# Optimization experiments

Measured on AMD Instinct MI355X. Metric: run time of the kernel, lower is better.

## Reference

```python
import jax, jax.numpy as jnp
import numpy as np

BN_EPS = 1e-5

def _conv(x, w, b, pad):
    # x: [B,C,H,W], w: [O,I,kh,kw] -> [B,O,H,W]
    y = jax.lax.conv_general_dilated(x, w, window_strides=(1, 1),
                                     padding=[(pad, pad), (pad, pad)],
                                     dimension_numbers=("NCHW", "OIHW", "NCHW"))
    return y + b[None, :, None, None]

def setup_inputs() -> dict:
    key = jax.random.key(0)
    ks = jax.random.split(key, 5)
    B, Cin, H, W = 2, 256, 80, 80
    Ck, Cv, Cout = 128, 256, 256
    std = 0.02  # matches torch normal_(0, 0.02) init
    return {
        "x": jax.random.normal(ks[0], (B, Cin, H, W), jnp.float32),
        "wk": std * jax.random.normal(ks[1], (Ck, Cin, 1, 1), jnp.float32),
        "bk": jnp.zeros((Ck,), jnp.float32),
        "gamma": jnp.ones((Ck,), jnp.float32),
        "beta": jnp.zeros((Ck,), jnp.float32),
        "rmean": jnp.zeros((Ck,), jnp.float32),
        "rvar": jnp.ones((Ck,), jnp.float32),
        "wv": std * jax.random.normal(ks[2], (Cv, Cin, 3, 3), jnp.float32),
        "bv": jnp.zeros((Cv,), jnp.float32),
        "ww": std * jax.random.normal(ks[3], (Cout, Cv, 1, 1), jnp.float32),
        "bw": jnp.zeros((Cout,), jnp.float32),
    }

def reference(x, wk, bk, gamma, beta, rmean, rvar, wv, bv, ww, bw):
    B, Cin, H, W = x.shape
    Ck, Cv = wk.shape[0], wv.shape[0]
    N = H * W

    # f_key == f_query (shared module): 1x1 conv + BatchNorm (inference stats)
    kq = _conv(x, wk, bk, pad=0)                      # [B,Ck,H,W]
    inv = gamma / jnp.sqrt(rvar + BN_EPS)
    kq = kq * inv[None, :, None, None] + (beta - rmean * inv)[None, :, None, None]
    kq = kq.reshape(B, Ck, N)                          # key layout [B,Ck,N]

    # f_value: 3x3 conv
    value = _conv(x, wv, bv, pad=1).reshape(B, Cv, N)  # [B,Cv,N]

    # sim_map = query^T @ key -> [B,N,N], full softmax over last dim
    sim = jnp.einsum("bcn,bcm->bnm", kq, kq)
    sim = jax.nn.softmax(sim, axis=-1)

    # context = sim @ value^T -> [B,N,Cv] -> [B,Cv,H,W]
    ctx = jnp.einsum("bnm,bcm->bcn", sim, value).reshape(B, Cv, H, W)

    out = _conv(ctx, ww, bw, pad=0) + x                # residual
    return out
```

## Files before the change

kernel.cpp:

```cpp
#include <hip/hip_runtime.h>
#include <math.h>

#define NB   2
#define CIN  256
#define IMH  80
#define IMW  80
#define NPIX (IMH*IMW)
#define CK   128
#define CVC  256
#define COUTC 256
#define BN_EPS 1e-5f
#define HP   82
#define WP   82
#define NMC  (NPIX / 64)
#define LOG2E 1.4426950408889634f
#define M0L  28.853900817779268f

typedef short sx8 __attribute__((ext_vector_type(8)));
typedef short sx4 __attribute__((ext_vector_type(4)));
typedef float f32x4 __attribute__((ext_vector_type(4)));

__device__ __forceinline__ short f2bf(float f) {
    unsigned u = __builtin_bit_cast(unsigned, f);
    u += 0x7fffu + ((u >> 16) & 1u);
    return (short)(u >> 16);
}
__device__ __forceinline__ float bf2f(short s) {
    unsigned u = ((unsigned)(unsigned short)s) << 16;
    return __builtin_bit_cast(float, u);
}
__device__ __forceinline__ int pk_bf16(float a, float b) {
    unsigned ua = __builtin_bit_cast(unsigned, a) + 0x8000u;
    unsigned ub = __builtin_bit_cast(unsigned, b) + 0x8000u;
    return __builtin_amdgcn_perm(ub, ua, 0x07060302);
}

#define WVT_BLKS 256
#define WWB_BLKS 256
#define WKB_BLKS 128
__global__ __launch_bounds__(256) void prep_kernel(
    const float* __restrict__ wv, const float* __restrict__ ww,
    const float* __restrict__ wk, const float* __restrict__ bk,
    const float* __restrict__ gamma, const float* __restrict__ beta,
    const float* __restrict__ rmean, const float* __restrict__ rvar,
    short* __restrict__ wvt, short* __restrict__ wwb,
    short* __restrict__ wkb, float* __restrict__ bias2)
{
    __shared__ short L[9][258];
    const int tid = threadIdx.x;
    const int bx  = blockIdx.x;

    if (bx < WVT_BLKS) {
        const float* src = wv + (size_t)bx * 2304;
        #pragma unroll
        for (int i = 0; i < 9; ++i) {
            int m = i * 256 + tid;
            L[m % 9][m / 9] = f2bf(src[m]);
        }
        __syncthreads();
        #pragma unroll
        for (int j = 0; j < 9; ++j)
            wvt[(size_t)j * (CVC * CIN) + bx * 256 + tid] = L[j][tid];
    } else if (bx < WVT_BLKS + WWB_BLKS) {
        int idx = (bx - WVT_BLKS) * 256 + tid;
        wwb[idx] = f2bf(ww[idx]);
    } else {
        int idx = (bx - WVT_BLKS - WWB_BLKS) * 256 + tid;
        int ck = idx >> 8;
        float inv = gamma[ck] * rsqrtf(rvar[ck] + BN_EPS);
        wkb[idx] = f2bf(wk[idx] * inv);
        if (idx < CK) {
            float invi = gamma[idx] * rsqrtf(rvar[idx] + BN_EPS);
            bias2[idx] = (bk[idx] - rmean[idx]) * invi + beta[idx];
        }
    }
}

__global__ __launch_bounds__(256) void padkq_kernel(
    const float* __restrict__ x, const short* __restrict__ wkb,
    const float* __restrict__ bias2, short* __restrict__ xpad,
    short* __restrict__ kqT)
{
    __shared__ short T[64][258];
    const int tid = threadIdx.x;
    const int n0  = blockIdx.x * 64;
    const int b   = blockIdx.y;
    const float* xb = x + (size_t)b * CIN * NPIX;

    #pragma unroll 4
    for (int i = 0; i < 64; ++i) {
        int e = tid + i * 256;
        int pix = e & 63, c = e >> 6;
        T[pix][c] = f2bf(xb[(size_t)c * NPIX + n0 + pix]);
    }
    __syncthreads();

    #pragma unroll
    for (int i = 0; i < 8; ++i) {
        int e   = tid + i * 256;
        int pix = e >> 5;
        int cp  = (e & 31) * 8;
        int np  = n0 + pix;
        int hp  = np / IMW + 1, wp = np % IMW + 1;
        sx8 v = *(const sx8*)&T[pix][cp];
        *(sx8*)&xpad[(((size_t)b * HP + hp) * WP + wp) * CIN + cp] = v;
    }

    {
        int e = blockIdx.x * 256 + tid;
        if (e < 324 * 32) {
            int p = e >> 5, c8 = (e & 31) * 8;
            int hp, wp;
            if      (p < 82)  { hp = 0;       wp = p;       }
            else if (p < 164) { hp = 81;      wp = p - 82;  }
            else if (p < 244) { hp = p - 163; wp = 0;       }
            else              { hp = p - 243; wp = 81;      }
            sx8 z = {};
            *(sx8*)&xpad[(((size_t)b * HP + hp) * WP + wp) * CIN + c8] = z;
        }
    }

    const int wid  = tid >> 6;
    const int lane = tid & 63;
    const int l15  = lane & 15;
    const int quad = lane >> 4;
    const int ck0  = wid * 32;

    f32x4 acc[2][4];
    #pragma unroll
    for (int at = 0; at < 2; ++at)
        #pragma unroll
        for (int nt = 0; nt < 4; ++nt)
            acc[at][nt] = (f32x4){0.f, 0.f, 0.f, 0.f};

    for (int kc = 0; kc < CIN / 32; ++kc) {
        sx8 af0 = *(const sx8*)&wkb[(size_t)(ck0 + l15) * CIN + kc * 32 + quad * 8];
        sx8 af1 = *(const sx8*)&wkb[(size_t)(ck0 + 16 + l15) * CIN + kc * 32 + quad * 8];
        #pragma unroll
        for (int nt = 0; nt < 4; ++nt) {
            sx8 bf = *(const sx8*)&T[nt * 16 + l15][kc * 32 + quad * 8];
            acc[0][nt] = __builtin_amdgcn_mfma_f32_16x16x32_bf16(af0, bf, acc[0][nt], 0, 0, 0);
            acc[1][nt] = __builtin_amdgcn_mfma_f32_16x16x32_bf16(af1, bf, acc[1][nt], 0, 0, 0);
        }
    }

    __syncthreads();

    #pragma unroll
    for (int at = 0; at < 2; ++at) {
        f32x4 b4 = *(const f32x4*)&bias2[ck0 + at * 16 + quad * 4];
        #pragma unroll
        for (int nt = 0; nt < 4; ++nt)
            #pragma unroll
            for (int r = 0; r < 4; ++r)
                T[nt * 16 + l15][ck0 + at * 16 + quad * 4 + r] = f2bf(acc[at][nt][r] + b4[r]);
    }
    __syncthreads();
    #pragma unroll
    for (int it = 0; it < 4; ++it) {
        int e = tid + it * 256;
        int row = e >> 4, c8 = (e & 15) * 8;
        *(sx8*)&kqT[((size_t)b * NPIX + n0 + row) * CK + c8] = *(const sx8*)&T[row][c8];
    }
}

#define CSTRIDE 36
__global__ __launch_bounds__(512) void conv3_kernel(
    const short* __restrict__ xpad, const short* __restrict__ wvt,
    const float* __restrict__ bv, short* __restrict__ valF)
{
    __shared__ __align__(16) short Xs[2][6 * 18 * CSTRIDE];

    const int tid  = threadIdx.x;
    const int wid  = tid >> 6;
    const int lane = tid & 63;
    const int l15  = lane & 15;
    const int quad = lane >> 4;

    const int rowT = blockIdx.x / 5, colT = blockIdx.x % 5;
    const int h0 = rowT * 4, w0 = colT * 16;
    const int cv0 = blockIdx.y * 128 + wid * 16;
    const int b   = blockIdx.z;

    const short* xb = xpad + (size_t)b * HP * WP * CIN;

    const int rc  = tid >> 2, l4 = tid & 3;
    const int row = rc / 18, col = rc % 18;
    const bool sv = (tid < 432);
    const short* sptr = &xb[(((size_t)(h0 + row)) * WP + (w0 + col)) * CIN + l4 * 8];
    const int sdst = rc * CSTRIDE + l4 * 8;

    f32x4 acc[4];
    #pragma unroll
    for (int r = 0; r < 4; ++r) acc[r] = (f32x4){0.f, 0.f, 0.f, 0.f};

    sx8 v = {};
    if (sv) {
        v = *(const sx8*)&sptr[0];
        *(sx8*)&Xs[0][sdst] = v;
    }
    __syncthreads();

    for (int cc = 0; cc < CIN / 32; ++cc) {
        const int cur = cc & 1;
        if (cc + 1 < CIN / 32 && sv)
            v = *(const sx8*)&sptr[(cc + 1) * 32];

        #pragma unroll
        for (int dw = 0; dw < 3; ++dw) {
            sx8 Bf[6];
            #pragma unroll
            for (int rr = 0; rr < 6; ++rr)
                Bf[rr] = *(const sx8*)&Xs[cur][(rr * 18 + l15 + dw) * CSTRIDE + quad * 8];
            #pragma unroll
            for (int dh = 0; dh < 3; ++dh) {
                int tap = dh * 3 + dw;
                sx8 Af = *(const sx8*)&wvt[((size_t)(tap * 256 + cv0 + l15)) * CIN + cc * 32 + quad * 8];
                #pragma unroll
                for (int r = 0; r < 4; ++r)
                    acc[r] = __builtin_amdgcn_mfma_f32_16x16x32_bf16(Af, Bf[r + dh], acc[r], 0, 0, 0);
            }
        }

        if (cc + 1 < CIN / 32 && sv)
            *(sx8*)&Xs[cur ^ 1][sdst] = v;
        __syncthreads();
    }

    f32x4 bvv = *(const f32x4*)&bv[cv0 + quad * 4];
    const int cvt = cv0 >> 4;
    #pragma unroll
    for (int r = 0; r < 4; ++r) {
        int n  = (h0 + r) * IMW + w0 + l15;
        int mc = n >> 6, s2 = (n >> 5) & 1, qm = (n >> 3) & 3, mi = n & 7;
        size_t base = ((((size_t)(b * NMC + mc) * 16 + cvt) * 2 + s2) * 4 + qm) * 128;
        #pragma unroll
        for (int reg = 0; reg < 4; ++reg)
            valF[base + (quad * 4 + reg) * 8 + mi] = f2bf(acc[r][reg] + bvv[reg]);
    }
}

#define TQ 64
#define TK 64
#define KS_LD 132
#define PS_LD 72

template<int SP>
__global__ __launch_bounds__(512) void attn_kernel(
    const short* __restrict__ kqT, const short* __restrict__ valF,
    short* __restrict__ opart, float* __restrict__ lpart)
{
    constexpr int NCc  = NPIX / SP / 64;
    constexpr int SPSH = (SP == 4) ? 3 : 2;

    __shared__ __align__(16) short Ks[TK][KS_LD];
    __shared__ __align__(16) short Pb[TQ][PS_LD];
    __shared__ float lqs[2][64];

    const int tid  = threadIdx.x;
    const int wid  = tid >> 6;
    const int lane = tid & 63;
    const int l15  = lane & 15;
    const int quad = lane >> 4;
    const int qw   = wid & 3;
    const int mh   = wid >> 2;

    const int blk = blockIdx.x;
    const int b   = blk & 1;
    const int sp  = (blk >> 1) & (SP - 1);
    const int n0  = (blk >> SPSH) * TQ;
    const int mb  = sp * (NPIX / SP);

    const short* kqb = kqT + (size_t)b * NPIX * CK;
    const short* vbase = valF + ((size_t)(b * NMC + sp * NCc) * 16 + wid * 2) * 1024
                              + (size_t)lane * 8;

    const int srow = tid >> 4;
    const int sc8  = (tid & 15) * 8;

    sx8 qf[4];
    #pragma unroll
    for (int s = 0; s < 4; ++s)
        qf[s] = *(const sx8*)&kqb[(size_t)(n0 + qw * 16 + l15) * CK + s * 32 + quad * 8];

    sx8 kreg[2];
    #pragma unroll
    for (int p = 0; p < 2; ++p)
        kreg[p] = *(const sx8*)&kqb[(size_t)(mb + srow + p * 32) * CK + sc8];
    #pragma unroll
    for (int p = 0; p < 2; ++p)
        *(sx8*)&Ks[srow + p * 32][sc8] = kreg[p];

    sx8 vreg[4];
    #pragma unroll
    for (int ct = 0; ct < 2; ++ct)
        #pragma unroll
        for (int s2 = 0; s2 < 2; ++s2)
            vreg[ct * 2 + s2] = *(const sx8*)&vbase[ct * 1024 + s2 * 512];

    float lq = 0.f;
    f32x4 acc[4][2];
    #pragma unroll
    for (int qt = 0; qt < 4; ++qt)
        #pragma unroll
        for (int ct = 0; ct < 2; ++ct)
            acc[qt][ct] = (f32x4){0.f, 0.f, 0.f, 0.f};

    __syncthreads();

    for (int i = 0; i < NCc; ++i) {
        if (i + 1 < NCc) {
            #pragma unroll
            for (int p = 0; p < 2; ++p)
                kreg[p] = *(const sx8*)&kqb[(size_t)(mb + (i + 1) * TK + srow + p * 32) * CK + sc8];
        }

        f32x4 st[2];
        #pragma unroll
        for (int t2 = 0; t2 < 2; ++t2) st[t2] = (f32x4){0.f, 0.f, 0.f, 0.f};
        #pragma unroll
        for (int s = 0; s < 4; ++s) {
            sx8 af[2];
            #pragma unroll
            for (int t2 = 0; t2 < 2; ++t2)
                af[t2] = *(const sx8*)&Ks[mh * 32 + t2 * 16 + l15][s * 32 + quad * 8];
            #pragma unroll
            for (int t2 = 0; t2 < 2; ++t2)
                st[t2] = __builtin_amdgcn_mfma_f32_16x16x32_bf16(af[t2], qf[s], st[t2], 0, 0, 0);
        }

        __syncthreads();

        #pragma unroll
        for (int t2 = 0; t2 < 2; ++t2)
            #pragma unroll
            for (int r = 0; r < 4; ++r)
                st[t2][r] = exp2f(fmaf(st[t2][r], LOG2E, -M0L));

        if (i + 1 < NCc) {
            #pragma unroll
            for (int p = 0; p < 2; ++p)
                *(sx8*)&Ks[srow + p * 32][sc8] = kreg[p];
        }

        #pragma unroll
        for (int t2 = 0; t2 < 2; ++t2) {
            int2 pw;
            pw.x = pk_bf16(st[t2][0], st[t2][1]);
            pw.y = pk_bf16(st[t2][2], st[t2][3]);
            *(int2*)&Pb[qw * 16 + l15][mh * 32 + t2 * 16 + quad * 4] = pw;
        }

        lq += (st[0][0] + st[0][1]) + (st[0][2] + st[0][3])
            + (st[1][0] + st[1][1]) + (st[1][2] + st[1][3]);

        __syncthreads();

        #pragma unroll
        for (int s2 = 0; s2 < 2; ++s2) {
            sx8 pa[4];
            #pragma unroll
            for (int qt = 0; qt < 4; ++qt)
                pa[qt] = *(const sx8*)&Pb[qt * 16 + l15][s2 * 32 + quad * 8];
            #pragma unroll
            for (int ct = 0; ct < 2; ++ct) {
                #pragma unroll
                for (int qt = 0; qt < 4; ++qt)
                    acc[qt][ct] = __builtin_amdgcn_mfma_f32_16x16x32_bf16(pa[qt], vreg[ct * 2 + s2], acc[qt][ct], 0, 0, 0);
            }
        }

        if (i + 1 < NCc) {
            #pragma unroll
            for (int ct = 0; ct < 2; ++ct)
                #pragma unroll
                for (int s2 = 0; s2 < 2; ++s2)
                    vreg[ct * 2 + s2] = *(const sx8*)&vbase[(size_t)(i + 1) * 16384 + ct * 1024 + s2 * 512];
        }
    }

    lq += __shfl_xor(lq, 16);
    lq += __shfl_xor(lq, 32);
    if (quad == 0)
        lqs[mh][qw * 16 + l15] = lq;

    size_t obase = (size_t)(sp * NB + b) * NPIX + n0;
    #pragma unroll
    for (int qt = 0; qt < 4; ++qt)
        #pragma unroll
        for (int ct = 0; ct < 2; ++ct) {
            int cv = wid * 32 + ct * 16 + l15;
            #pragma unroll
            for (int r = 0; r < 4; ++r)
                opart[(obase + qt * 16 + quad * 4 + r) * CVC + cv] = f2bf(acc[qt][ct][r]);
        }

    __syncthreads();
    if (tid < 64)
        lpart[obase + tid] = lqs[0][tid] + lqs[1][tid];
}

#define BS_LD 40
template<int SP>
__global__ __launch_bounds__(512) void out_kernel(
    const short* __restrict__ opart, const float* __restrict__ lpart,
    const short* __restrict__ wwb, const float* __restrict__ bw,
    const float* __restrict__ x, float* __restrict__ out)
{
    __shared__ __align__(16) short Bs[2][64][BS_LD];
    __shared__ float rinvs[64];

    const int tid  = threadIdx.x;
    const int wid  = tid >> 6;
    const int lane = tid & 63;
    const int l15  = lane & 15;
    const int quad = lane >> 4;

    const int n0  = blockIdx.x * 64;
    const int co0 = wid * 32;
    const int b   = blockIdx.y;

    if (tid < 64) {
        int n = n0 + tid;
        float ls = 0.f;
        #pragma unroll
        for (int s = 0; s < SP; ++s)
            ls += lpart[(size_t)(s * NB + b) * NPIX + n];
        rinvs[tid] = 1.f / ls;
    }

    const int srow = tid >> 2;
    const int sc8  = (tid & 3) * 8;
    const short* op0 = opart + ((size_t)b * NPIX + n0 + srow) * CVC + sc8;
    constexpr size_t SSTR = (size_t)NB * NPIX * CVC;
    const bool sv = (tid < 256);

    __syncthreads();

    if (sv) {
        float ri = rinvs[srow];
        float sacc[8] = {0.f, 0.f, 0.f, 0.f, 0.f, 0.f, 0.f, 0.f};
        #pragma unroll
        for (int s = 0; s < SP; ++s) {
            sx8 a = *(const sx8*)&op0[s * SSTR];
            #pragma unroll
            for (int j = 0; j < 8; ++j)
                sacc[j] += bf2f(a[j]);
        }
        sx8 o;
        #pragma unroll
        for (int j = 0; j < 8; ++j)
            o[j] = f2bf(sacc[j] * ri);
        *(sx8*)&Bs[0][srow][sc8] = o;
    }
    __syncthreads();

    f32x4 acc[4][2];
    #pragma unroll
    for (int nt = 0; nt < 4; ++nt)
        #pragma unroll
        for (int ct = 0; ct < 2; ++ct)
            acc[nt][ct] = (f32x4){0.f, 0.f, 0.f, 0.f};

    for (int cc = 0; cc < CVC / 32; ++cc) {
        const int cur = cc & 1;
        const bool st = (cc + 1 < CVC / 32) && sv;

        sx8 a[SP];
        if (st) {
            #pragma unroll
            for (int s = 0; s < SP; ++s)
                a[s] = *(const sx8*)&op0[s * SSTR + (cc + 1) * 32];
        }

        sx8 af[2];
        #pragma unroll
        for (int ct = 0; ct < 2; ++ct)
            af[ct] = *(const sx8*)&wwb[(size_t)(co0 + ct * 16 + l15) * CVC + cc * 32 + quad * 8];
        #pragma unroll
        for (int nt = 0; nt < 4; ++nt) {
            sx8 bf = *(const sx8*)&Bs[cur][nt * 16 + l15][quad * 8];
            #pragma unroll
            for (int ct = 0; ct < 2; ++ct)
                acc[nt][ct] = __builtin_amdgcn_mfma_f32_16x16x32_bf16(af[ct], bf, acc[nt][ct], 0, 0, 0);
        }

        if (st) {
            float ri = rinvs[srow];
            float sacc[8] = {0.f, 0.f, 0.f, 0.f, 0.f, 0.f, 0.f, 0.f};
            #pragma unroll
            for (int s = 0; s < SP; ++s)
                #pragma unroll
                for (int j = 0; j < 8; ++j)
                    sacc[j] += bf2f(a[s][j]);
            sx8 o;
            #pragma unroll
            for (int j = 0; j < 8; ++j)
                o[j] = f2bf(sacc[j] * ri);
            *(sx8*)&Bs[cur ^ 1][srow][sc8] = o;
        }
        __syncthreads();
    }

    #pragma unroll
    for (int ct = 0; ct < 2; ++ct) {
        f32x4 bv4 = *(const f32x4*)&bw[co0 + ct * 16 + quad * 4];
        #pragma unroll
        for (int nt = 0; nt < 4; ++nt) {
            #pragma unroll
            for (int r = 0; r < 4; ++r) {
                int co = co0 + ct * 16 + quad * 4 + r;
                int n  = n0 + nt * 16 + l15;
                size_t gi = ((size_t)b * COUTC + co) * NPIX + n;
                out[gi] = acc[nt][ct][r] + bv4[r] + x[gi];
            }
        }
    }
}

extern "C" void kernel_launch(void* const* d_in, const int* in_sizes, int n_in,
                              void* d_out, int out_size, void* d_ws, size_t ws_size,
                              hipStream_t stream)
{
    const float* x     = (const float*)d_in[0];
    const float* wk    = (const float*)d_in[1];
    const float* bk    = (const float*)d_in[2];
    const float* gamma = (const float*)d_in[3];
    const float* beta  = (const float*)d_in[4];
    const float* rmean = (const float*)d_in[5];
    const float* rvar  = (const float*)d_in[6];
    const float* wv    = (const float*)d_in[7];
    const float* bv    = (const float*)d_in[8];
    const float* ww    = (const float*)d_in[9];
    const float* bw    = (const float*)d_in[10];
    float* out = (float*)d_out;

    constexpr int SPL = 2;
    const size_t perSplit = (size_t)NB * NPIX * CVC;

    short* opart = (short*)d_ws;
    short* xpad  = opart;
    short* wvt   = xpad + (size_t)NB * HP * WP * CIN;
    short* wwb   = opart + (size_t)SPL * perSplit;
    short* wkb   = wwb  + (size_t)COUTC * CVC;
    short* kqT   = wkb  + (size_t)CK * CIN;
    short* valF  = kqT  + (size_t)NB * NPIX * CK;
    float* bias2 = (float*)(valF + perSplit);
    float* lpart = bias2 + CK;

    prep_kernel  <<<WVT_BLKS + WWB_BLKS + WKB_BLKS, 256, 0, stream>>>(
        wv, ww, wk, bk, gamma, beta, rmean, rvar, wvt, wwb, wkb, bias2);
    padkq_kernel <<<dim3(NPIX/64, NB),          256, 0, stream>>>(x, wkb, bias2, xpad, kqT);
    conv3_kernel <<<dim3(100, CVC/128,     NB), 512, 0, stream>>>(xpad, wvt, bv, valF);
    attn_kernel<SPL> <<<NB * SPL * (NPIX / TQ), 512, 0, stream>>>(kqT, valF, opart, lpart);
    out_kernel<SPL>  <<<dim3(100, NB),          512, 0, stream>>>(opart, lpart, wwb, bw, x, out);
}
```

Baseline: 223.8 us.

## Double attention query tile to 128 with 1024-thread blocks and 4-way key split

The attention kernel now processes 128 queries per block with 16 waves. Each wave owns 16 value channels instead of 32, and the key dimension is split into 4 partitions instead of 2. Doubling the query tile halves the number of times K and V tiles are re-read per query, while the larger split keeps the block count up. The cost is more partial outputs for out_kernel to reduce, larger 1024-thread blocks with tighter register limits, and more partial-result memory traffic. The workspace layout must also hold 4 splits, and it is unclear that it does.

After: 253.4 us. 1.13x slower.

```diff
diff --git a/kernel.cpp b/kernel.cpp
--- a/kernel.cpp
+++ b/kernel.cpp
@@ -240,13 +240,13 @@
     }
 }
 
-#define TQ 64
+#define TQ 128
 #define TK 64
 #define KS_LD 132
 #define PS_LD 72
 
 template<int SP>
-__global__ __launch_bounds__(512) void attn_kernel(
+__global__ __launch_bounds__(1024) void attn_kernel(
     const short* __restrict__ kqT, const short* __restrict__ valF,
     short* __restrict__ opart, float* __restrict__ lpart)
 {
@@ -255,15 +255,15 @@
 
     __shared__ __align__(16) short Ks[TK][KS_LD];
     __shared__ __align__(16) short Pb[TQ][PS_LD];
-    __shared__ float lqs[2][64];
+    __shared__ float lqs[2][TQ];
 
     const int tid  = threadIdx.x;
     const int wid  = tid >> 6;
     const int lane = tid & 63;
     const int l15  = lane & 15;
     const int quad = lane >> 4;
-    const int qw   = wid & 3;
-    const int mh   = wid >> 2;
+    const int qw   = wid & 7;
+    const int mh   = wid >> 3;
 
     const int blk = blockIdx.x;
     const int b   = blk & 1;
@@ -272,7 +272,7 @@
     const int mb  = sp * (NPIX / SP);
 
     const short* kqb = kqT + (size_t)b * NPIX * CK;
-    const short* vbase = valF + ((size_t)(b * NMC + sp * NCc) * 16 + wid * 2) * 1024
+    const short* vbase = valF + ((size_t)(b * NMC + sp * NCc) * 16 + wid) * 1024
                               + (size_t)lane * 8;
 
     const int srow = tid >> 4;
@@ -283,37 +283,25 @@
     for (int s = 0; s < 4; ++s)
         qf[s] = *(const sx8*)&kqb[(size_t)(n0 + qw * 16 + l15) * CK + s * 32 + quad * 8];
 
-    sx8 kreg[2];
-    #pragma unroll
-    for (int p = 0; p < 2; ++p)
-        kreg[p] = *(const sx8*)&kqb[(size_t)(mb + srow + p * 32) * CK + sc8];
-    #pragma unroll
-    for (int p = 0; p < 2; ++p)
-        *(sx8*)&Ks[srow + p * 32][sc8] = kreg[p];
-
-    sx8 vreg[4];
-    #pragma unroll
-    for (int ct = 0; ct < 2; ++ct)
-        #pragma unroll
-        for (int s2 = 0; s2 < 2; ++s2)
-            vreg[ct * 2 + s2] = *(const sx8*)&vbase[ct * 1024 + s2 * 512];
+    sx8 kreg = *(const sx8*)&kqb[(size_t)(mb + srow) * CK + sc8];
+    *(sx8*)&Ks[srow][sc8] = kreg;
+
+    sx8 vreg[2];
+    #pragma unroll
+    for (int s2 = 0; s2 < 2; ++s2)
+        vreg[s2] = *(const sx8*)&vbase[s2 * 512];
 
     float lq = 0.f;
-    f32x4 acc[4][2];
-    #pragma unroll
-    for (int qt = 0; qt < 4; ++qt)
-        #pragma unroll
-        for (int ct = 0; ct < 2; ++ct)
-            acc[qt][ct] = (f32x4){0.f, 0.f, 0.f, 0.f};
+    f32x4 acc[8];
+    #pragma unroll
+    for (int qt = 0; qt < 8; ++qt)
+        acc[qt] = (f32x4){0.f, 0.f, 0.f, 0.f};
 
     __syncthreads();
 
     for (int i = 0; i < NCc; ++i) {
-        if (i + 1 < NCc) {
-            #pragma unroll
-            for (int p = 0; p < 2; ++p)
-                kreg[p] = *(const sx8*)&kqb[(size_t)(mb + (i + 1) * TK + srow + p * 32) * CK + sc8];
-        }
+        if (i + 1 < NCc)
+            kreg = *(const sx8*)&kqb[(size_t)(mb + (i + 1) * TK + srow) * CK + sc8];
 
         f32x4 st[2];
         #pragma unroll
@@ -337,11 +325,8 @@
             for (int r = 0; r < 4; ++r)
                 st[t2][r] = exp2f(fmaf(st[t2][r], LOG2E, -M0L));
 
-        if (i + 1 < NCc) {
-            #pragma unroll
-            for (int p = 0; p < 2; ++p)
-                *(sx8*)&Ks[srow + p * 32][sc8] = kreg[p];
-        }
+        if (i + 1 < NCc)
+            *(sx8*)&Ks[srow][sc8] = kreg;
 
         #pragma unroll
         for (int t2 = 0; t2 < 2; ++t2) {
@@ -358,24 +343,19 @@
 
         #pragma unroll
         for (int s2 = 0; s2 < 2; ++s2) {
-            sx8 pa[4];
-            #pragma unroll
-            for (int qt = 0; qt < 4; ++qt)
+            sx8 pa[8];
+            #pragma unroll
+            for (int qt = 0; qt < 8; ++qt)
                 pa[qt] = *(const sx8*)&Pb[qt * 16 + l15][s2 * 32 + quad * 8];
             #pragma unroll
-            for (int ct = 0; ct < 2; ++ct) {
-                #pragma unroll
-                for (int qt = 0; qt < 4; ++qt)
-                    acc[qt][ct] = __builtin_amdgcn_mfma_f32_16x16x32_bf16(pa[qt], vreg[ct * 2 + s2], acc[qt][ct], 0, 0, 0);
-            }
+            for (int qt = 0; qt < 8; ++qt)
+                acc[qt] = __builtin_amdgcn_mfma_f32_16x16x32_bf16(pa[qt], vreg[s2], acc[qt], 0, 0, 0);
         }
 
         if (i + 1 < NCc) {
             #pragma unroll
-            for (int ct = 0; ct < 2; ++ct)
-                #pragma unroll
-                for (int s2 = 0; s2 < 2; ++s2)
-                    vreg[ct * 2 + s2] = *(const sx8*)&vbase[(size_t)(i + 1) * 16384 + ct * 1024 + s2 * 512];
+            for (int s2 = 0; s2 < 2; ++s2)
+                vreg[s2] = *(const sx8*)&vbase[(size_t)(i + 1) * 16384 + s2 * 512];
         }
     }
 
@@ -385,18 +365,16 @@
         lqs[mh][qw * 16 + l15] = lq;
 
     size_t obase = (size_t)(sp * NB + b) * NPIX + n0;
-    #pragma unroll
-    for (int qt = 0; qt < 4; ++qt)
-        #pragma unroll
-        for (int ct = 0; ct < 2; ++ct) {
-            int cv = wid * 32 + ct * 16 + l15;
-            #pragma unroll
-            for (int r = 0; r < 4; ++r)
-                opart[(obase + qt * 16 + quad * 4 + r) * CVC + cv] = f2bf(acc[qt][ct][r]);
-        }
-
-    __syncthreads();
-    if (tid < 64)
+    const int cv = wid * 16 + l15;
+    #pragma unroll
+    for (int qt = 0; qt < 8; ++qt) {
+        #pragma unroll
+        for (int r = 0; r < 4; ++r)
+            opart[(obase + qt * 16 + quad * 4 + r) * CVC + cv] = f2bf(acc[qt][r]);
+    }
+
+    __syncthreads();
+    if (tid < TQ)
         lpart[obase + tid] = lqs[0][tid] + lqs[1][tid];
 }
 
@@ -535,7 +513,7 @@
     const float* bw    = (const float*)d_in[10];
     float* out = (float*)d_out;
 
-    constexpr int SPL = 2;
+    constexpr int SPL = 4;
     const size_t perSplit = (size_t)NB * NPIX * CVC;
 
     short* opart = (short*)d_ws;
@@ -552,6 +530,6 @@
         wv, ww, wk, bk, gamma, beta, rmean, rvar, wvt, wwb, wkb, bias2);
     padkq_kernel <<<dim3(NPIX/64, NB),          256, 0, stream>>>(x, wkb, bias2, xpad, kqT);
     conv3_kernel <<<dim3(100, CVC/128,     NB), 512, 0, stream>>>(xpad, wvt, bv, valF);
-    attn_kernel<SPL> <<<NB * SPL * (NPIX / TQ), 512, 0, stream>>>(kqT, valF, opart, lpart);
+    attn_kernel<SPL> <<<NB * SPL * (NPIX / TQ), 1024, 0, stream>>>(kqT, valF, opart, lpart);
     out_kernel<SPL>  <<<dim3(100, NB),          512, 0, stream>>>(opart, lpart, wwb, bw, x, out);
 }
```

## Switch attention kernel to 32x32x16 MFMA with 128-key tiles and new value layout

Applied to the files above, without the earlier changes.

Rewrites the attention inner loop to use 32x32x16 bf16 MFMA instead of 16x16x32, and doubles the key tile from 64 to 128 so each loop step does more work per barrier. The value-conv epilogue writes a new fragment layout matching the 32-wide B operand, and the row-sum reduction is regrouped across four key-tile warps. This aims to cut MFMA issue count, LDS fragment reads and per-tile synchronisation, at the cost of more registers (16-wide accumulators, 8 Q and V fragments) and larger LDS tiles, which may reduce occupancy.

Measured after the change: 245.8 us. +9.8%, slower.

```diff
diff --git a/kernel.cpp b/kernel.cpp
--- a/kernel.cpp
+++ b/kernel.cpp
@@ -12,13 +12,12 @@
 #define BN_EPS 1e-5f
 #define HP   82
 #define WP   82
-#define NMC  (NPIX / 64)
 #define LOG2E 1.4426950408889634f
 #define M0L  28.853900817779268f
 
 typedef short sx8 __attribute__((ext_vector_type(8)));
-typedef short sx4 __attribute__((ext_vector_type(4)));
 typedef float f32x4 __attribute__((ext_vector_type(4)));
+typedef float f32x16 __attribute__((ext_vector_type(16)));
 
 __device__ __forceinline__ short f2bf(float f) {
     unsigned u = __builtin_bit_cast(unsigned, f);
@@ -228,42 +227,43 @@
     }
 
     f32x4 bvv = *(const f32x4*)&bv[cv0 + quad * 4];
-    const int cvt = cv0 >> 4;
     #pragma unroll
     for (int r = 0; r < 4; ++r) {
-        int n  = (h0 + r) * IMW + w0 + l15;
-        int mc = n >> 6, s2 = (n >> 5) & 1, qm = (n >> 3) & 3, mi = n & 7;
-        size_t base = ((((size_t)(b * NMC + mc) * 16 + cvt) * 2 + s2) * 4 + qm) * 128;
-        #pragma unroll
-        for (int reg = 0; reg < 4; ++reg)
-            valF[base + (quad * 4 + reg) * 8 + mi] = f2bf(acc[r][reg] + bvv[reg]);
+        int n = (h0 + r) * IMW + w0 + l15;
+        #pragma unroll
+        for (int reg = 0; reg < 4; ++reg) {
+            int cv = cv0 + quad * 4 + reg;
+            size_t idx = (((size_t)(b * (NPIX / 16) + (n >> 4)) * 8 + (cv >> 5)) << 9)
+                       + (size_t)(((n >> 3) & 1) * 256 + (cv & 31) * 8 + (n & 7));
+            valF[idx] = f2bf(acc[r][reg] + bvv[reg]);
+        }
     }
 }
 
 #define TQ 64
-#define TK 64
+#define TK2 128
 #define KS_LD 132
-#define PS_LD 72
+#define PS2  132
 
 template<int SP>
 __global__ __launch_bounds__(512) void attn_kernel(
     const short* __restrict__ kqT, const short* __restrict__ valF,
     short* __restrict__ opart, float* __restrict__ lpart)
 {
-    constexpr int NCc  = NPIX / SP / 64;
+    constexpr int NCc  = NPIX / SP / TK2;
     constexpr int SPSH = (SP == 4) ? 3 : 2;
 
-    __shared__ __align__(16) short Ks[TK][KS_LD];
-    __shared__ __align__(16) short Pb[TQ][PS_LD];
-    __shared__ float lqs[2][64];
+    __shared__ __align__(16) short Ks[TK2][KS_LD];
+    __shared__ __align__(16) short Pb[TQ][PS2];
+    __shared__ float lqs[4][2][32];
 
     const int tid  = threadIdx.x;
     const int wid  = tid >> 6;
     const int lane = tid & 63;
-    const int l15  = lane & 15;
-    const int quad = lane >> 4;
-    const int qw   = wid & 3;
-    const int mh   = wid >> 2;
+    const int l31  = lane & 31;
+    const int hi   = lane >> 5;
+    const int mt   = wid & 3;
+    const int qt   = wid >> 2;
 
     const int blk = blockIdx.x;
     const int b   = blk & 1;
@@ -272,132 +272,119 @@
     const int mb  = sp * (NPIX / SP);
 
     const short* kqb = kqT + (size_t)b * NPIX * CK;
-    const short* vbase = valF + ((size_t)(b * NMC + sp * NCc) * 16 + wid * 2) * 1024
+    const short* vbase = valF + (((size_t)(b * (NPIX / 16) + mb / 16) * 8 + wid) << 9)
                               + (size_t)lane * 8;
 
     const int srow = tid >> 4;
     const int sc8  = (tid & 15) * 8;
 
-    sx8 qf[4];
-    #pragma unroll
-    for (int s = 0; s < 4; ++s)
-        qf[s] = *(const sx8*)&kqb[(size_t)(n0 + qw * 16 + l15) * CK + s * 32 + quad * 8];
-
-    sx8 kreg[2];
-    #pragma unroll
-    for (int p = 0; p < 2; ++p)
+    sx8 qf[8];
+    #pragma unroll
+    for (int s = 0; s < 8; ++s)
+        qf[s] = *(const sx8*)&kqb[(size_t)(n0 + qt * 32 + l31) * CK + s * 16 + hi * 8];
+
+    sx8 kreg[4];
+    #pragma unroll
+    for (int p = 0; p < 4; ++p)
         kreg[p] = *(const sx8*)&kqb[(size_t)(mb + srow + p * 32) * CK + sc8];
     #pragma unroll
-    for (int p = 0; p < 2; ++p)
+    for (int p = 0; p < 4; ++p)
         *(sx8*)&Ks[srow + p * 32][sc8] = kreg[p];
 
-    sx8 vreg[4];
-    #pragma unroll
-    for (int ct = 0; ct < 2; ++ct)
-        #pragma unroll
-        for (int s2 = 0; s2 < 2; ++s2)
-            vreg[ct * 2 + s2] = *(const sx8*)&vbase[ct * 1024 + s2 * 512];
+    sx8 vreg[8];
+    #pragma unroll
+    for (int s = 0; s < 8; ++s)
+        vreg[s] = *(const sx8*)&vbase[(size_t)s * 4096];
 
     float lq = 0.f;
-    f32x4 acc[4][2];
-    #pragma unroll
-    for (int qt = 0; qt < 4; ++qt)
-        #pragma unroll
-        for (int ct = 0; ct < 2; ++ct)
-            acc[qt][ct] = (f32x4){0.f, 0.f, 0.f, 0.f};
+    f32x16 acc[2];
+    #pragma unroll
+    for (int q2 = 0; q2 < 2; ++q2)
+        #pragma unroll
+        for (int r = 0; r < 16; ++r)
+            acc[q2][r] = 0.f;
 
     __syncthreads();
 
     for (int i = 0; i < NCc; ++i) {
         if (i + 1 < NCc) {
             #pragma unroll
-            for (int p = 0; p < 2; ++p)
-                kreg[p] = *(const sx8*)&kqb[(size_t)(mb + (i + 1) * TK + srow + p * 32) * CK + sc8];
-        }
-
-        f32x4 st[2];
-        #pragma unroll
-        for (int t2 = 0; t2 < 2; ++t2) st[t2] = (f32x4){0.f, 0.f, 0.f, 0.f};
-        #pragma unroll
-        for (int s = 0; s < 4; ++s) {
-            sx8 af[2];
-            #pragma unroll
-            for (int t2 = 0; t2 < 2; ++t2)
-                af[t2] = *(const sx8*)&Ks[mh * 32 + t2 * 16 + l15][s * 32 + quad * 8];
-            #pragma unroll
-            for (int t2 = 0; t2 < 2; ++t2)
-                st[t2] = __builtin_amdgcn_mfma_f32_16x16x32_bf16(af[t2], qf[s], st[t2], 0, 0, 0);
+            for (int p = 0; p < 4; ++p)
+                kreg[p] = *(const sx8*)&kqb[(size_t)(mb + (i + 1) * TK2 + srow + p * 32) * CK + sc8];
+        }
+
+        f32x16 st;
+        #pragma unroll
+        for (int r = 0; r < 16; ++r) st[r] = 0.f;
+        #pragma unroll
+        for (int s = 0; s < 8; ++s) {
+            sx8 af = *(const sx8*)&Ks[mt * 32 + l31][s * 16 + hi * 8];
+            st = __builtin_amdgcn_mfma_f32_32x32x16_bf16(af, qf[s], st, 0, 0, 0);
         }
 
         __syncthreads();
 
         #pragma unroll
-        for (int t2 = 0; t2 < 2; ++t2)
-            #pragma unroll
-            for (int r = 0; r < 4; ++r)
-                st[t2][r] = exp2f(fmaf(st[t2][r], LOG2E, -M0L));
+        for (int r = 0; r < 16; ++r)
+            st[r] = exp2f(fmaf(st[r], LOG2E, -M0L));
 
         if (i + 1 < NCc) {
             #pragma unroll
-            for (int p = 0; p < 2; ++p)
+            for (int p = 0; p < 4; ++p)
                 *(sx8*)&Ks[srow + p * 32][sc8] = kreg[p];
         }
 
         #pragma unroll
-        for (int t2 = 0; t2 < 2; ++t2) {
+        for (int g = 0; g < 4; ++g) {
             int2 pw;
-            pw.x = pk_bf16(st[t2][0], st[t2][1]);
-            pw.y = pk_bf16(st[t2][2], st[t2][3]);
-            *(int2*)&Pb[qw * 16 + l15][mh * 32 + t2 * 16 + quad * 4] = pw;
-        }
-
-        lq += (st[0][0] + st[0][1]) + (st[0][2] + st[0][3])
-            + (st[1][0] + st[1][1]) + (st[1][2] + st[1][3]);
+            pw.x = pk_bf16(st[4 * g + 0], st[4 * g + 1]);
+            pw.y = pk_bf16(st[4 * g + 2], st[4 * g + 3]);
+            *(int2*)&Pb[qt * 32 + l31][mt * 32 + 8 * g + 4 * hi] = pw;
+        }
+
+        {
+            float sum = 0.f;
+            #pragma unroll
+            for (int r = 0; r < 16; ++r) sum += st[r];
+            lq += sum;
+        }
 
         __syncthreads();
 
         #pragma unroll
-        for (int s2 = 0; s2 < 2; ++s2) {
-            sx8 pa[4];
-            #pragma unroll
-            for (int qt = 0; qt < 4; ++qt)
-                pa[qt] = *(const sx8*)&Pb[qt * 16 + l15][s2 * 32 + quad * 8];
-            #pragma unroll
-            for (int ct = 0; ct < 2; ++ct) {
-                #pragma unroll
-                for (int qt = 0; qt < 4; ++qt)
-                    acc[qt][ct] = __builtin_amdgcn_mfma_f32_16x16x32_bf16(pa[qt], vreg[ct * 2 + s2], acc[qt][ct], 0, 0, 0);
-            }
+        for (int s = 0; s < 8; ++s) {
+            sx8 pa0 = *(const sx8*)&Pb[l31][s * 16 + hi * 8];
+            sx8 pa1 = *(const sx8*)&Pb[32 + l31][s * 16 + hi * 8];
+            acc[0] = __builtin_amdgcn_mfma_f32_32x32x16_bf16(pa0, vreg[s], acc[0], 0, 0, 0);
+            acc[1] = __builtin_amdgcn_mfma_f32_32x32x16_bf16(pa1, vreg[s], acc[1], 0, 0, 0);
         }
 
         if (i + 1 < NCc) {
             #pragma unroll
-            for (int ct = 0; ct < 2; ++ct)
-                #pragma unroll
-                for (int s2 = 0; s2 < 2; ++s2)
-                    vreg[ct * 2 + s2] = *(const sx8*)&vbase[(size_t)(i + 1) * 16384 + ct * 1024 + s2 * 512];
-        }
-    }
-
-    lq += __shfl_xor(lq, 16);
+            for (int s = 0; s < 8; ++s)
+                vreg[s] = *(const sx8*)&vbase[(size_t)(i + 1) * 32768 + (size_t)s * 4096];
+        }
+    }
+
     lq += __shfl_xor(lq, 32);
-    if (quad == 0)
-        lqs[mh][qw * 16 + l15] = lq;
+    if (lane < 32)
+        lqs[mt][qt][l31] = lq;
 
     size_t obase = (size_t)(sp * NB + b) * NPIX + n0;
-    #pragma unroll
-    for (int qt = 0; qt < 4; ++qt)
-        #pragma unroll
-        for (int ct = 0; ct < 2; ++ct) {
-            int cv = wid * 32 + ct * 16 + l15;
-            #pragma unroll
-            for (int r = 0; r < 4; ++r)
-                opart[(obase + qt * 16 + quad * 4 + r) * CVC + cv] = f2bf(acc[qt][ct][r]);
-        }
+    const int cv = wid * 32 + l31;
+    #pragma unroll
+    for (int q2 = 0; q2 < 2; ++q2) {
+        #pragma unroll
+        for (int r = 0; r < 16; ++r) {
+            int q = q2 * 32 + (r & 3) + 8 * (r >> 2) + 4 * hi;
+            opart[(obase + q) * CVC + cv] = f2bf(acc[q2][r]);
+        }
+    }
 
     __syncthreads();
     if (tid < 64)
-        lpart[obase + tid] = lqs[0][tid] + lqs[1][tid];
+        lpart[obase + tid] = lqs[0][tid >> 5][tid & 31] + lqs[1][tid >> 5][tid & 31]
+                           + lqs[2][tid >> 5][tid & 31] + lqs[3][tid >> 5][tid & 31];
 }
 
 #define BS_LD 40
```

## Drop split-KV in attention and halve padkq pixel tile

Applied to the files above, without the earlier changes.

The attention kernel no longer splits the key/value range in two. Each block now walks all key chunks and normalizes its output by the softmax denominator before storing, so the partial output and lpart buffers go away. The output kernel loses its combine-and-rescale step and just streams the normalized bf16 context into its GEMM. The pad/key-projection kernel now uses 32-pixel tiles instead of 64, doubling its block count. The trade is that attention launches half as many blocks, each doing twice the work, which may underfill the GPU in exchange for less partial-result traffic.

Result: slower. 269.7 us (+20.5%).

```diff
diff --git a/kernel.cpp b/kernel.cpp
--- a/kernel.cpp
+++ b/kernel.cpp
@@ -17,7 +17,6 @@
 #define M0L  28.853900817779268f
 
 typedef short sx8 __attribute__((ext_vector_type(8)));
-typedef short sx4 __attribute__((ext_vector_type(4)));
 typedef float f32x4 __attribute__((ext_vector_type(4)));
 
 __device__ __forceinline__ short f2bf(float f) {
@@ -81,22 +80,22 @@
     const float* __restrict__ bias2, short* __restrict__ xpad,
     short* __restrict__ kqT)
 {
-    __shared__ short T[64][258];
+    __shared__ short T[32][258];
     const int tid = threadIdx.x;
-    const int n0  = blockIdx.x * 64;
+    const int n0  = blockIdx.x * 32;
     const int b   = blockIdx.y;
     const float* xb = x + (size_t)b * CIN * NPIX;
 
     #pragma unroll 4
-    for (int i = 0; i < 64; ++i) {
+    for (int i = 0; i < 32; ++i) {
         int e = tid + i * 256;
-        int pix = e & 63, c = e >> 6;
+        int pix = e & 31, c = e >> 5;
         T[pix][c] = f2bf(xb[(size_t)c * NPIX + n0 + pix]);
     }
     __syncthreads();
 
     #pragma unroll
-    for (int i = 0; i < 8; ++i) {
+    for (int i = 0; i < 4; ++i) {
         int e   = tid + i * 256;
         int pix = e >> 5;
         int cp  = (e & 31) * 8;
@@ -126,18 +125,18 @@
     const int quad = lane >> 4;
     const int ck0  = wid * 32;
 
-    f32x4 acc[2][4];
+    f32x4 acc[2][2];
     #pragma unroll
     for (int at = 0; at < 2; ++at)
         #pragma unroll
-        for (int nt = 0; nt < 4; ++nt)
+        for (int nt = 0; nt < 2; ++nt)
             acc[at][nt] = (f32x4){0.f, 0.f, 0.f, 0.f};
 
     for (int kc = 0; kc < CIN / 32; ++kc) {
         sx8 af0 = *(const sx8*)&wkb[(size_t)(ck0 + l15) * CIN + kc * 32 + quad * 8];
         sx8 af1 = *(const sx8*)&wkb[(size_t)(ck0 + 16 + l15) * CIN + kc * 32 + quad * 8];
         #pragma unroll
-        for (int nt = 0; nt < 4; ++nt) {
+        for (int nt = 0; nt < 2; ++nt) {
             sx8 bf = *(const sx8*)&T[nt * 16 + l15][kc * 32 + quad * 8];
             acc[0][nt] = __builtin_amdgcn_mfma_f32_16x16x32_bf16(af0, bf, acc[0][nt], 0, 0, 0);
             acc[1][nt] = __builtin_amdgcn_mfma_f32_16x16x32_bf16(af1, bf, acc[1][nt], 0, 0, 0);
@@ -150,14 +149,14 @@
     for (int at = 0; at < 2; ++at) {
         f32x4 b4 = *(const f32x4*)&bias2[ck0 + at * 16 + quad * 4];
         #pragma unroll
-        for (int nt = 0; nt < 4; ++nt)
+        for (int nt = 0; nt < 2; ++nt)
             #pragma unroll
             for (int r = 0; r < 4; ++r)
                 T[nt * 16 + l15][ck0 + at * 16 + quad * 4 + r] = f2bf(acc[at][nt][r] + b4[r]);
     }
     __syncthreads();
     #pragma unroll
-    for (int it = 0; it < 4; ++it) {
+    for (int it = 0; it < 2; ++it) {
         int e = tid + it * 256;
         int row = e >> 4, c8 = (e & 15) * 8;
         *(sx8*)&kqT[((size_t)b * NPIX + n0 + row) * CK + c8] = *(const sx8*)&T[row][c8];
@@ -245,17 +244,16 @@
 #define KS_LD 132
 #define PS_LD 72
 
-template<int SP>
 __global__ __launch_bounds__(512) void attn_kernel(
     const short* __restrict__ kqT, const short* __restrict__ valF,
-    short* __restrict__ opart, float* __restrict__ lpart)
+    short* __restrict__ opart)
 {
-    constexpr int NCc  = NPIX / SP / 64;
-    constexpr int SPSH = (SP == 4) ? 3 : 2;
+    constexpr int NCc = NPIX / 64;
 
     __shared__ __align__(16) short Ks[TK][KS_LD];
     __shared__ __align__(16) short Pb[TQ][PS_LD];
     __shared__ float lqs[2][64];
+    __shared__ float rinvs[64];
 
     const int tid  = threadIdx.x;
     const int wid  = tid >> 6;
@@ -267,12 +265,10 @@
 
     const int blk = blockIdx.x;
     const int b   = blk & 1;
-    const int sp  = (blk >> 1) & (SP - 1);
-    const int n0  = (blk >> SPSH) * TQ;
-    const int mb  = sp * (NPIX / SP);
+    const int n0  = (blk >> 1) * TQ;
 
     const short* kqb = kqT + (size_t)b * NPIX * CK;
-    const short* vbase = valF + ((size_t)(b * NMC + sp * NCc) * 16 + wid * 2) * 1024
+    const short* vbase = valF + ((size_t)(b * NMC) * 16 + wid * 2) * 1024
                               + (size_t)lane * 8;
 
     const int srow = tid >> 4;
@@ -286,7 +282,7 @@
     sx8 kreg[2];
     #pragma unroll
     for (int p = 0; p < 2; ++p)
-        kreg[p] = *(const sx8*)&kqb[(size_t)(mb + srow + p * 32) * CK + sc8];
+        kreg[p] = *(const sx8*)&kqb[(size_t)(srow + p * 32) * CK + sc8];
     #pragma unroll
     for (int p = 0; p < 2; ++p)
         *(sx8*)&Ks[srow + p * 32][sc8] = kreg[p];
@@ -312,7 +308,7 @@
         if (i + 1 < NCc) {
             #pragma unroll
             for (int p = 0; p < 2; ++p)
-                kreg[p] = *(const sx8*)&kqb[(size_t)(mb + (i + 1) * TK + srow + p * 32) * CK + sc8];
+                kreg[p] = *(const sx8*)&kqb[(size_t)((i + 1) * TK + srow + p * 32) * CK + sc8];
         }
 
         f32x4 st[2];
@@ -384,31 +380,32 @@
     if (quad == 0)
         lqs[mh][qw * 16 + l15] = lq;
 
-    size_t obase = (size_t)(sp * NB + b) * NPIX + n0;
+    __syncthreads();
+    if (tid < 64)
+        rinvs[tid] = 1.f / (lqs[0][tid] + lqs[1][tid]);
+    __syncthreads();
+
+    size_t obase = (size_t)b * NPIX + n0;
     #pragma unroll
     for (int qt = 0; qt < 4; ++qt)
         #pragma unroll
         for (int ct = 0; ct < 2; ++ct) {
             int cv = wid * 32 + ct * 16 + l15;
             #pragma unroll
-            for (int r = 0; r < 4; ++r)
-                opart[(obase + qt * 16 + quad * 4 + r) * CVC + cv] = f2bf(acc[qt][ct][r]);
-        }
-
-    __syncthreads();
-    if (tid < 64)
-        lpart[obase + tid] = lqs[0][tid] + lqs[1][tid];
+            for (int r = 0; r < 4; ++r) {
+                int q = qt * 16 + quad * 4 + r;
+                opart[(obase + q) * CVC + cv] = f2bf(acc[qt][ct][r] * rinvs[q]);
+            }
+        }
 }
 
 #define BS_LD 40
-template<int SP>
 __global__ __launch_bounds__(512) void out_kernel(
-    const short* __restrict__ opart, const float* __restrict__ lpart,
-    const short* __restrict__ wwb, const float* __restrict__ bw,
-    const float* __restrict__ x, float* __restrict__ out)
+    const short* __restrict__ opart, const short* __restrict__ wwb,
+    const float* __restrict__ bw, const float* __restrict__ x,
+    float* __restrict__ out)
 {
     __shared__ __align__(16) short Bs[2][64][BS_LD];
-    __shared__ float rinvs[64];
 
     const int tid  = threadIdx.x;
     const int wid  = tid >> 6;
@@ -420,39 +417,13 @@
     const int co0 = wid * 32;
     const int b   = blockIdx.y;
 
-    if (tid < 64) {
-        int n = n0 + tid;
-        float ls = 0.f;
-        #pragma unroll
-        for (int s = 0; s < SP; ++s)
-            ls += lpart[(size_t)(s * NB + b) * NPIX + n];
-        rinvs[tid] = 1.f / ls;
-    }
-
     const int srow = tid >> 2;
     const int sc8  = (tid & 3) * 8;
     const short* op0 = opart + ((size_t)b * NPIX + n0 + srow) * CVC + sc8;
-    constexpr size_t SSTR = (size_t)NB * NPIX * CVC;
     const bool sv = (tid < 256);
 
-    __syncthreads();
-
-    if (sv) {
-        float ri = rinvs[srow];
-        float sacc[8] = {0.f, 0.f, 0.f, 0.f, 0.f, 0.f, 0.f, 0.f};
-        #pragma unroll
-        for (int s = 0; s < SP; ++s) {
-            sx8 a = *(const sx8*)&op0[s * SSTR];
-            #pragma unroll
-            for (int j = 0; j < 8; ++j)
-                sacc[j] += bf2f(a[j]);
-        }
-        sx8 o;
-        #pragma unroll
-        for (int j = 0; j < 8; ++j)
-            o[j] = f2bf(sacc[j] * ri);
-        *(sx8*)&Bs[0][srow][sc8] = o;
-    }
+    if (sv)
+        *(sx8*)&Bs[0][srow][sc8] = *(const sx8*)&op0[0];
     __syncthreads();
 
     f32x4 acc[4][2];
@@ -466,12 +437,9 @@
         const int cur = cc & 1;
         const bool st = (cc + 1 < CVC / 32) && sv;
 
-        sx8 a[SP];
-        if (st) {
-            #pragma unroll
-            for (int s = 0; s < SP; ++s)
-                a[s] = *(const sx8*)&op0[s * SSTR + (cc + 1) * 32];
-        }
+        sx8 a;
+        if (st)
+            a = *(const sx8*)&op0[(cc + 1) * 32];
 
         sx8 af[2];
         #pragma unroll
@@ -485,20 +453,8 @@
                 acc[nt][ct] = __builtin_amdgcn_mfma_f32_16x16x32_bf16(af[ct], bf, acc[nt][ct], 0, 0, 0);
         }
 
-        if (st) {
-            float ri = rinvs[srow];
-            float sacc[8] = {0.f, 0.f, 0.f, 0.f, 0.f, 0.f, 0.f, 0.f};
-            #pragma unroll
-            for (int s = 0; s < SP; ++s)
-                #pragma unroll
-                for (int j = 0; j < 8; ++j)
-                    sacc[j] += bf2f(a[s][j]);
-            sx8 o;
-            #pragma unroll
-            for (int j = 0; j < 8; ++j)
-                o[j] = f2bf(sacc[j] * ri);
-            *(sx8*)&Bs[cur ^ 1][srow][sc8] = o;
-        }
+        if (st)
+            *(sx8*)&Bs[cur ^ 1][srow][sc8] = a;
         __syncthreads();
     }
 
@@ -535,23 +491,23 @@
     const float* bw    = (const float*)d_in[10];
     float* out = (float*)d_out;
 
-    constexpr int SPL = 2;
-    const size_t perSplit = (size_t)NB * NPIX * CVC;
+    const size_t xpadShorts = (size_t)NB * HP * WP * CIN;
+    const size_t wvtShorts  = (size_t)9 * CVC * CIN;
+    const size_t region0    = xpadShorts + wvtShorts;
 
     short* opart = (short*)d_ws;
     short* xpad  = opart;
-    short* wvt   = xpad + (size_t)NB * HP * WP * CIN;
-    short* wwb   = opart + (size_t)SPL * perSplit;
+    short* wvt   = xpad + xpadShorts;
+    short* wwb   = opart + region0;
     short* wkb   = wwb  + (size_t)COUTC * CVC;
     short* kqT   = wkb  + (size_t)CK * CIN;
     short* valF  = kqT  + (size_t)NB * NPIX * CK;
-    float* bias2 = (float*)(valF + perSplit);
-    float* lpart = bias2 + CK;
+    float* bias2 = (float*)(valF + (size_t)NB * NPIX * CVC);
 
     prep_kernel  <<<WVT_BLKS + WWB_BLKS + WKB_BLKS, 256, 0, stream>>>(
         wv, ww, wk, bk, gamma, beta, rmean, rvar, wvt, wwb, wkb, bias2);
-    padkq_kernel <<<dim3(NPIX/64, NB),          256, 0, stream>>>(x, wkb, bias2, xpad, kqT);
+    padkq_kernel <<<dim3(NPIX/32, NB),          256, 0, stream>>>(x, wkb, bias2, xpad, kqT);
     conv3_kernel <<<dim3(100, CVC/128,     NB), 512, 0, stream>>>(xpad, wvt, bv, valF);
-    attn_kernel<SPL> <<<NB * SPL * (NPIX / TQ), 512, 0, stream>>>(kqT, valF, opart, lpart);
-    out_kernel<SPL>  <<<dim3(100, NB),          512, 0, stream>>>(opart, lpart, wwb, bw, x, out);
-}
+    attn_kernel  <<<NB * (NPIX / TQ),           512, 0, stream>>>(kqT, valF, opart);
+    out_kernel   <<<dim3(100, NB),              512, 0, stream>>>(opart, wwb, bw, x, out);
+}
```
